# Kernel optimization log

Measured on AMD Instinct MI355X. Metric: run time of the kernel, lower is better.

Reference implementation:

```python
import jax, jax.numpy as jnp
import numpy as np

B, T, C = 4, 4096, 1024
HEAD = 128


def setup_inputs() -> dict:
    key = jax.random.key(0)
    k0, k1, k2, k3 = jax.random.split(key, 4)
    x = jax.random.normal(k0, (B, T, C), dtype=jnp.float32)
    # bias-free linear weights, stored as (in, out) so y = x @ W
    Wk = jax.random.normal(k1, (C, HEAD), dtype=jnp.float32) * (C ** -0.5)
    Wq = jax.random.normal(k2, (C, HEAD), dtype=jnp.float32) * (C ** -0.5)
    Wv = jax.random.normal(k3, (C, HEAD), dtype=jnp.float32) * (C ** -0.5)
    return {"x": x, "Wk": Wk, "Wq": Wq, "Wv": Wv}


def reference(x, Wk, Wq, Wv):
    Bx, Tx, Cx = x.shape
    k = x @ Wk            # [B,T,H]
    q = x @ Wq            # [B,T,H]
    v = x @ Wv            # [B,T,H]
    # NOTE: original code scales by C**-0.5 where C = n_embd (input dim), not head_size
    scale = Cx ** -0.5
    wei = jnp.einsum("bqh,bkh->bqk", q, k) * scale        # [B,T,T]
    causal = jnp.arange(Tx)[:, None] >= jnp.arange(Tx)[None, :]
    wei = jnp.where(causal, wei, -jnp.inf)
    wei = jax.nn.softmax(wei, axis=-1)
    # dropout rate is 0.0 in the source -> identity
    return jnp.einsum("bqk,bkh->bqh", wei, v)             # [B,T,H]
```

## Files before the change

kernel.cpp:

```cpp
#include <hip/hip_runtime.h>


typedef __bf16 bf16;
typedef bf16 bf16x8 __attribute__((ext_vector_type(8)));
typedef bf16 bf16x4 __attribute__((ext_vector_type(4)));
typedef float f32x4 __attribute__((ext_vector_type(4)));

#define L2E 1.4426950408889634f
#define TSEQ 4096
#define CDIM 1024
#define HDIM 128
#define MROWS 16384

#define GLDS(g, l)                                              \
  __builtin_amdgcn_global_load_lds(                             \
      (__attribute__((address_space(1))) void*)(g),             \
      (__attribute__((address_space(3))) void*)(l), 16, 0, 0)

static __device__ inline unsigned pkbf(float a, float b) {
  union { bf16 h; unsigned short u; } ua, ub;
  ua.h = (bf16)a; ub.h = (bf16)b;
  return ((unsigned)ub.u << 16) | (unsigned)ua.u;
}

__global__ __launch_bounds__(256) void wt_prep(const float* __restrict__ Wq,
                                               const float* __restrict__ Wk,
                                               const float* __restrict__ Wv,
                                               bf16* __restrict__ WT) {
  const int mode = blockIdx.y;
  const float* W = (mode == 0) ? Wq : (mode == 1) ? Wk : Wv;
  const int idx = blockIdx.x * 256 + threadIdx.x;
  const int n = idx >> 10;
  const int k = idx & 1023;
  WT[(size_t)mode * 131072 + idx] = (bf16)W[(size_t)k * HDIM + n];
}

__global__ __launch_bounds__(256) void qkv_gemm(const float* __restrict__ x,
                                                const bf16* __restrict__ WT,
                                                bf16* __restrict__ qb,
                                                bf16* __restrict__ kb,
                                                bf16* __restrict__ vT) {
  __shared__ __attribute__((aligned(16))) bf16 a_tile[128 * 32];
  __shared__ __attribute__((aligned(16))) bf16 b_tile[128 * 32];
  const int tid = threadIdx.x;
  const int wid = tid >> 6;
  const int lane = tid & 63;
  const int lr = lane & 15;
  const int lg = lane >> 4;
  const int wr = wid >> 1;
  const int wc = wid & 1;
  const int mode = blockIdx.y;
  const int m0 = blockIdx.x * 128;
  const bf16* wt = WT + (size_t)mode * 131072;

  int rowA[2], col8[2];
#pragma unroll
  for (int g = 0; g < 2; ++g) {
    const int idx8 = g * 256 + tid;
    rowA[g] = idx8 >> 2;
    col8[g] = (idx8 & 3) * 8;
  }

  f32x4 acc[4][4] = {};

  float4 fA[2][2];
  bf16x8 fB[2];
#pragma unroll
  for (int g = 0; g < 2; ++g) {
    const float* src = x + (size_t)(m0 + rowA[g]) * CDIM + col8[g];
    fA[g][0] = *(const float4*)src;
    fA[g][1] = *(const float4*)(src + 4);
    fB[g] = *(const bf16x8*)(wt + (size_t)rowA[g] * CDIM + col8[g]);
  }

#pragma unroll 1
  for (int kt = 0; kt < 32; ++kt) {
    __syncthreads();
#pragma unroll
    for (int g = 0; g < 2; ++g) {
      bf16x8 av;
      av[0] = (bf16)fA[g][0].x; av[1] = (bf16)fA[g][0].y;
      av[2] = (bf16)fA[g][0].z; av[3] = (bf16)fA[g][0].w;
      av[4] = (bf16)fA[g][1].x; av[5] = (bf16)fA[g][1].y;
      av[6] = (bf16)fA[g][1].z; av[7] = (bf16)fA[g][1].w;
      *(bf16x8*)&a_tile[rowA[g] * 32 + col8[g]] = av;
      *(bf16x8*)&b_tile[rowA[g] * 32 + col8[g]] = fB[g];
    }
    __syncthreads();
    if (kt + 1 < 32) {
#pragma unroll
      for (int g = 0; g < 2; ++g) {
        const float* src = x + (size_t)(m0 + rowA[g]) * CDIM + (kt + 1) * 32 + col8[g];
        fA[g][0] = *(const float4*)src;
        fA[g][1] = *(const float4*)(src + 4);
        fB[g] = *(const bf16x8*)(wt + (size_t)rowA[g] * CDIM + (kt + 1) * 32 + col8[g]);
      }
    }
    bf16x8 af[4], bfr[4];
#pragma unroll
    for (int r = 0; r < 4; ++r)
      af[r] = *(const bf16x8*)&a_tile[(wr * 64 + r * 16 + lr) * 32 + lg * 8];
#pragma unroll
    for (int c = 0; c < 4; ++c)
      bfr[c] = *(const bf16x8*)&b_tile[(wc * 64 + c * 16 + lr) * 32 + lg * 8];
#pragma unroll
    for (int r = 0; r < 4; ++r)
#pragma unroll
      for (int c = 0; c < 4; ++c)
        acc[r][c] = __builtin_amdgcn_mfma_f32_16x16x32_bf16(af[r], bfr[c], acc[r][c], 0, 0, 0);
  }

  if (mode < 2) {
    bf16* dst = (mode == 0) ? qb : kb;
    const float sc = (mode == 0) ? 0.03125f : 1.0f;
#pragma unroll
    for (int r = 0; r < 4; ++r)
#pragma unroll
      for (int c = 0; c < 4; ++c)
#pragma unroll
        for (int j = 0; j < 4; ++j) {
          const int row = m0 + wr * 64 + r * 16 + lg * 4 + j;
          const int col = wc * 64 + c * 16 + lr;
          dst[(size_t)row * HDIM + col] = (bf16)(acc[r][c][j] * sc);
        }
  } else {
#pragma unroll
    for (int r = 0; r < 4; ++r)
#pragma unroll
      for (int c = 0; c < 4; ++c) {
        const int row0 = m0 + wr * 64 + r * 16 + lg * 4;
        const int col = wc * 64 + c * 16 + lr;
        bf16x4 pv;
        pv[0] = (bf16)acc[r][c][0]; pv[1] = (bf16)acc[r][c][1];
        pv[2] = (bf16)acc[r][c][2]; pv[3] = (bf16)acc[r][c][3];
        *(bf16x4*)(vT + (size_t)(row0 >> 6) * 8192 + col * 64 + (row0 & 63)) = pv;
      }
  }
}

__global__ __launch_bounds__(512, 4) void attn_part(const bf16* __restrict__ qg,
                                                    const bf16* __restrict__ kb,
                                                    const bf16* __restrict__ vT,
                                                    bf16* __restrict__ po,
                                                    float* __restrict__ pm,
                                                    float* __restrict__ pl,
                                                    int cshift, int maxc) {
  __shared__ __attribute__((aligned(16))) char kv_lds[2][32768];
  __shared__ __attribute__((aligned(16))) bf16 p_lds[8][16][64];
  const int tid = threadIdx.x;
  const int wid = tid >> 6;
  const int lane = tid & 63;
  const int lr = lane & 15;
  const int lg = lane >> 4;

  int bx = blockIdx.x, c = blockIdx.y, b = blockIdx.z;
  if (maxc == 8) {
    const int p = blockIdx.x + 32 * (blockIdx.y + 8 * blockIdx.z);
    const int xcd = p & 7;
    const int s = p >> 3;
    const int combo = s >> 5;
    bx = s & 31;
    b = combo;
    c = (combo < 2) ? xcd : 7 - xcd;
  }

  const int qbase = bx * 128;
  const int kv0 = c << cshift;
  if (kv0 >= qbase + 128) return;
  const int kvend = min(kv0 + (1 << cshift), qbase + 128);
  const int nt = (kvend - kv0) >> 6;
  const int qr0 = qbase + wid * 16;
  const int grp = bx * 8 + wid;
  const size_t qrow = (size_t)b * TSEQ + qr0;

  const int wbase = wid * 2048;
  int ksrc[2], vsrc[2];
#pragma unroll
  for (int i = 0; i < 2; ++i) {
    const int o = wbase + i * 1024 + lane * 16;
    const int rk = o >> 8;
    ksrc[i] = rk * 256 + ((o & 255) ^ ((rk & 7) << 4));
    const int rv = o >> 7;
    vsrc[i] = rv * 128 + ((o & 127) ^ ((rv & 7) << 4));
  }
  const char* kgb = (const char*)kb + (size_t)b * TSEQ * 256;
  const char* vgb = (const char*)vT + (size_t)b * TSEQ * 256;

  const int msk = (lr & 7) << 4;
  const int m30 = (lr & 3) << 4;
  const int m6 = (lr & 4) << 4;
  const int lgx = (lg * 16) ^ m30;
  const int kreadA = lr * 256 + lgx + m6;
  const int kreadB = lr * 256 + lgx + (64 ^ m6);
  const int vreadA = 16384 + lr * 128 + lgx + m6;
  const int vreadB = 16384 + lr * 128 + lgx + (64 ^ m6);

  bf16x8 qf[4];
#pragma unroll
  for (int d = 0; d < 4; ++d)
    qf[d] = *(const bf16x8*)(qg + (qrow + lr) * HDIM + d * 32 + lg * 8);

  f32x4 o_[8] = {};
  float m_ = -1e30f, l_ = 0.0f;

  {
    const char* ks = kgb + (size_t)kv0 * 256;
    const char* vs = vgb + (size_t)kv0 * 256;
#pragma unroll
    for (int i = 0; i < 2; ++i) {
      GLDS(ks + ksrc[i], &kv_lds[0][wbase + i * 1024]);
      GLDS(vs + vsrc[i], &kv_lds[0][16384 + wbase + i * 1024]);
    }
  }
  __syncthreads();

  int cur = 0;
  for (int t = 0; t < nt; ++t) {
    const int kvt = kv0 + (t << 6);
    if (t + 1 < nt) {
      const char* ks = kgb + (size_t)(kvt + 64) * 256;
      const char* vs = vgb + (size_t)(kvt + 64) * 256;
#pragma unroll
      for (int i = 0; i < 2; ++i) {
        GLDS(ks + ksrc[i], &kv_lds[cur ^ 1][wbase + i * 1024]);
        GLDS(vs + vsrc[i], &kv_lds[cur ^ 1][16384 + wbase + i * 1024]);
      }
    }
    if (kvt < qr0 + 16) {
      const char* kbuf = kv_lds[cur];
      f32x4 s[4] = {};
      __builtin_amdgcn_s_setprio(1);
#pragma unroll
      for (int nf = 0; nf < 4; ++nf) {
        const char* kb0 = kbuf + nf * 4096;
        bf16x8 kf;
        kf = *(const bf16x8*)(kb0 + kreadA);
        s[nf] = __builtin_amdgcn_mfma_f32_16x16x32_bf16(kf, qf[0], s[nf], 0, 0, 0);
        kf = *(const bf16x8*)(kb0 + kreadB);
        s[nf] = __builtin_amdgcn_mfma_f32_16x16x32_bf16(kf, qf[1], s[nf], 0, 0, 0);
        kf = *(const bf16x8*)(kb0 + kreadA + 128);
        s[nf] = __builtin_amdgcn_mfma_f32_16x16x32_bf16(kf, qf[2], s[nf], 0, 0, 0);
        kf = *(const bf16x8*)(kb0 + kreadB + 128);
        s[nf] = __builtin_amdgcn_mfma_f32_16x16x32_bf16(kf, qf[3], s[nf], 0, 0, 0);
      }
      __builtin_amdgcn_s_setprio(0);
      if (kvt + 63 >= qr0) {
        const int q = qr0 + lr;
#pragma unroll
        for (int nf = 0; nf < 4; ++nf)
#pragma unroll
          for (int j = 0; j < 4; ++j)
            if (kvt + nf * 16 + lg * 4 + j > q) s[nf][j] = -1e30f;
      }
      float rloc = fmaxf(fmaxf(s[0][0], s[0][1]), fmaxf(s[0][2], s[0][3]));
#pragma unroll
      for (int nf = 1; nf < 4; ++nf)
        rloc = fmaxf(rloc, fmaxf(fmaxf(s[nf][0], s[nf][1]), fmaxf(s[nf][2], s[nf][3])));
      if (!__all(rloc <= m_ + 8.0f)) {
        float rmax = fmaxf(rloc, __shfl_xor(rloc, 16));
        rmax = fmaxf(rmax, __shfl_xor(rmax, 32));
        const float mn = fmaxf(m_, rmax);
        const float al = exp2f((m_ - mn) * L2E);
        m_ = mn;
        l_ *= al;
#pragma unroll
        for (int o = 0; o < 8; ++o)
#pragma unroll
          for (int j = 0; j < 4; ++j) o_[o][j] *= al;
      }
      float rsum = 0.0f;
#pragma unroll
      for (int nf = 0; nf < 4; ++nf)
#pragma unroll
        for (int j = 0; j < 4; ++j) {
          s[nf][j] = exp2f((s[nf][j] - m_) * L2E);
          rsum += s[nf][j];
        }
      l_ += rsum;
      {
        char* pw = (char*)p_lds + wid * 2048 + lr * 128;
#pragma unroll
        for (int nf = 0; nf < 4; ++nf) {
          uint2 w2;
          w2.x = pkbf(s[nf][0], s[nf][1]); w2.y = pkbf(s[nf][2], s[nf][3]);
          *(uint2*)(pw + (((nf * 32) + lg * 8) ^ msk)) = w2;
        }
      }
      asm volatile("s_waitcnt lgkmcnt(0)" ::: "memory");
      __builtin_amdgcn_sched_barrier(0);
      const char* pr = (const char*)p_lds + wid * 2048 + lr * 128;
      bf16x8 pf0 = *(const bf16x8*)(pr + lgx + m6);
      bf16x8 pf1 = *(const bf16x8*)(pr + lgx + (64 ^ m6));
      __builtin_amdgcn_s_setprio(1);
#pragma unroll
      for (int o = 0; o < 8; ++o) {
        bf16x8 vf;
        vf = *(const bf16x8*)(kbuf + vreadA + o * 2048);
        o_[o] = __builtin_amdgcn_mfma_f32_16x16x32_bf16(vf, pf0, o_[o], 0, 0, 0);
        vf = *(const bf16x8*)(kbuf + vreadB + o * 2048);
        o_[o] = __builtin_amdgcn_mfma_f32_16x16x32_bf16(vf, pf1, o_[o], 0, 0, 0);
      }
      __builtin_amdgcn_s_setprio(0);
    }
    __syncthreads();
    cur ^= 1;
  }

  l_ += __shfl_xor(l_, 16);
  l_ += __shfl_xor(l_, 32);

  const size_t slot = (size_t)(b * 256 + grp) * maxc + c;
  bf16* pob = po + slot * (16 * HDIM);
#pragma unroll
  for (int o = 0; o < 8; ++o) {
    bf16x4 pv;
    pv[0] = (bf16)o_[o][0]; pv[1] = (bf16)o_[o][1];
    pv[2] = (bf16)o_[o][2]; pv[3] = (bf16)o_[o][3];
    *(bf16x4*)(pob + lr * HDIM + o * 16 + lg * 4) = pv;
  }
  if (lg == 0) {
    pm[slot * 16 + lr] = m_;
    pl[slot * 16 + lr] = l_;
  }
}

__global__ __launch_bounds__(256) void attn_merge(const bf16* __restrict__ po,
                                                  const float* __restrict__ pm,
                                                  const float* __restrict__ pl,
                                                  float* __restrict__ out,
                                                  int cshift, int maxc) {
  const int bg = blockIdx.x;
  const int g = bg & 255;
  const int nch = ((g << 4) >> cshift) + 1;
  const int row = threadIdx.x >> 4;
  const int d8 = (threadIdx.x & 15) * 8;
  const size_t slot0 = (size_t)bg * maxc;

  float M = -1e30f;
  for (int c = 0; c < nch; ++c) M = fmaxf(M, pm[(slot0 + c) * 16 + row]);
  float L = 0.0f;
  float acc[8] = {};
  for (int c = 0; c < nch; ++c) {
    const float w = exp2f((pm[(slot0 + c) * 16 + row] - M) * L2E);
    L += w * pl[(slot0 + c) * 16 + row];
    const bf16x8 v = *(const bf16x8*)(po + (slot0 + c) * (16 * HDIM) + row * HDIM + d8);
#pragma unroll
    for (int i = 0; i < 8; ++i) acc[i] += w * (float)v[i];
  }
  const float inv = 1.0f / L;
  f32x4 r0, r1;
#pragma unroll
  for (int i = 0; i < 4; ++i) { r0[i] = acc[i] * inv; r1[i] = acc[i + 4] * inv; }
  float* dst = out + (size_t)bg * (16 * HDIM) + row * HDIM + d8;
  *(f32x4*)dst = r0;
  *(f32x4*)(dst + 4) = r1;
}

extern "C" void kernel_launch(void* const* d_in, const int* in_sizes, int n_in,
                              void* d_out, int out_size, void* d_ws, size_t ws_size,
                              hipStream_t stream) {
  const float* x  = (const float*)d_in[0];
  const float* Wk = (const float*)d_in[1];
  const float* Wq = (const float*)d_in[2];
  const float* Wv = (const float*)d_in[3];
  float* out = (float*)d_out;

  char* ws = (char*)d_ws;
  bf16* qb = (bf16*)(ws);
  bf16* kb = (bf16*)(ws + 4194304);
  bf16* vT = (bf16*)(ws + 8388608);
  bf16* WT = (bf16*)(ws + 12582912);
  const size_t pbase = 13369344;

  int cshift, maxc;
  if (ws_size >= pbase + 8ull * 1024 * 4224) { cshift = 9;  maxc = 8; }
  else if (ws_size >= pbase + 4ull * 1024 * 4224) { cshift = 10; maxc = 4; }
  else { cshift = 12; maxc = 1; }
  bf16* po = (bf16*)(ws + pbase);
  float* pm = (float*)(ws + pbase + (size_t)maxc * 1024 * 16 * 128 * 2);
  float* pl = pm + (size_t)maxc * 1024 * 16;

  wt_prep<<<dim3(512, 3), 256, 0, stream>>>(Wq, Wk, Wv, WT);
  qkv_gemm<<<dim3(128, 3), 256, 0, stream>>>(x, WT, qb, kb, vT);
  attn_part<<<dim3(32, maxc, 4), 512, 0, stream>>>(qb, kb, vT, po, pm, pl, cshift, maxc);
  attn_merge<<<1024, 256, 0, stream>>>(po, pm, pl, out, cshift, maxc);
}
```

Baseline: 90.21 us.

## Fuse Q/K/V projections into one GEMM reading x once per tile

After: 96.61 us. 1.07x slower.

```diff
diff --git a/kernel.cpp b/kernel.cpp
--- a/kernel.cpp
+++ b/kernel.cpp
@@ -35,106 +35,88 @@
   WT[(size_t)mode * 131072 + idx] = (bf16)W[(size_t)k * HDIM + n];
 }
 
-__global__ __launch_bounds__(256) void qkv_gemm(const float* __restrict__ x,
-                                                const bf16* __restrict__ WT,
-                                                bf16* __restrict__ qb,
-                                                bf16* __restrict__ kb,
-                                                bf16* __restrict__ vT) {
-  __shared__ __attribute__((aligned(16))) bf16 a_tile[128 * 32];
-  __shared__ __attribute__((aligned(16))) bf16 b_tile[128 * 32];
+__global__ __launch_bounds__(512, 2) void qkv_fused(const float* __restrict__ x,
+                                                    const bf16* __restrict__ WT,
+                                                    bf16* __restrict__ qb,
+                                                    bf16* __restrict__ kb,
+                                                    bf16* __restrict__ vT) {
+  __shared__ __attribute__((aligned(16))) bf16 a_tile[64 * 32];
+  __shared__ __attribute__((aligned(16))) bf16 b_tile[384 * 32];
   const int tid = threadIdx.x;
   const int wid = tid >> 6;
   const int lane = tid & 63;
   const int lr = lane & 15;
   const int lg = lane >> 4;
-  const int wr = wid >> 1;
-  const int wc = wid & 1;
-  const int mode = blockIdx.y;
-  const int m0 = blockIdx.x * 128;
-  const bf16* wt = WT + (size_t)mode * 131072;
-
-  int rowA[2], col8[2];
-#pragma unroll
-  for (int g = 0; g < 2; ++g) {
-    const int idx8 = g * 256 + tid;
-    rowA[g] = idx8 >> 2;
-    col8[g] = (idx8 & 3) * 8;
-  }
-
-  f32x4 acc[4][4] = {};
-
-  float4 fA[2][2];
-  bf16x8 fB[2];
-#pragma unroll
-  for (int g = 0; g < 2; ++g) {
-    const float* src = x + (size_t)(m0 + rowA[g]) * CDIM + col8[g];
-    fA[g][0] = *(const float4*)src;
-    fA[g][1] = *(const float4*)(src + 4);
-    fB[g] = *(const bf16x8*)(wt + (size_t)rowA[g] * CDIM + col8[g]);
+  const int wr = wid >> 2;
+  const int wcg = wid & 3;
+  const int m0 = blockIdx.x * 64;
+
+  const int ra = tid >> 3;
+  const int ca = (tid & 7) * 4;
+  const int rb = tid >> 2;
+  const int cb = (tid & 3) * 8;
+
+  f32x4 acc[2][6] = {};
+  float4 a0;
+  bf16x8 fB[3];
+  {
+    a0 = *(const float4*)(x + (size_t)(m0 + ra) * CDIM + ca);
+#pragma unroll
+    for (int i = 0; i < 3; ++i)
+      fB[i] = *(const bf16x8*)(WT + (size_t)i * 131072 + rb * 1024 + cb);
   }
 
 #pragma unroll 1
   for (int kt = 0; kt < 32; ++kt) {
     __syncthreads();
-#pragma unroll
-    for (int g = 0; g < 2; ++g) {
-      bf16x8 av;
-      av[0] = (bf16)fA[g][0].x; av[1] = (bf16)fA[g][0].y;
-      av[2] = (bf16)fA[g][0].z; av[3] = (bf16)fA[g][0].w;
-      av[4] = (bf16)fA[g][1].x; av[5] = (bf16)fA[g][1].y;
-      av[6] = (bf16)fA[g][1].z; av[7] = (bf16)fA[g][1].w;
-      *(bf16x8*)&a_tile[rowA[g] * 32 + col8[g]] = av;
-      *(bf16x8*)&b_tile[rowA[g] * 32 + col8[g]] = fB[g];
+    {
+      bf16x4 av;
+      av[0] = (bf16)a0.x; av[1] = (bf16)a0.y; av[2] = (bf16)a0.z; av[3] = (bf16)a0.w;
+      *(bf16x4*)&a_tile[ra * 32 + ca] = av;
+#pragma unroll
+      for (int i = 0; i < 3; ++i)
+        *(bf16x8*)&b_tile[(i * 128 + rb) * 32 + cb] = fB[i];
     }
     __syncthreads();
     if (kt + 1 < 32) {
-#pragma unroll
-      for (int g = 0; g < 2; ++g) {
-        const float* src = x + (size_t)(m0 + rowA[g]) * CDIM + (kt + 1) * 32 + col8[g];
-        fA[g][0] = *(const float4*)src;
-        fA[g][1] = *(const float4*)(src + 4);
-        fB[g] = *(const bf16x8*)(wt + (size_t)rowA[g] * CDIM + (kt + 1) * 32 + col8[g]);
-      }
-    }
-    bf16x8 af[4], bfr[4];
-#pragma unroll
-    for (int r = 0; r < 4; ++r)
-      af[r] = *(const bf16x8*)&a_tile[(wr * 64 + r * 16 + lr) * 32 + lg * 8];
-#pragma unroll
-    for (int c = 0; c < 4; ++c)
-      bfr[c] = *(const bf16x8*)&b_tile[(wc * 64 + c * 16 + lr) * 32 + lg * 8];
-#pragma unroll
-    for (int r = 0; r < 4; ++r)
-#pragma unroll
-      for (int c = 0; c < 4; ++c)
-        acc[r][c] = __builtin_amdgcn_mfma_f32_16x16x32_bf16(af[r], bfr[c], acc[r][c], 0, 0, 0);
-  }
-
-  if (mode < 2) {
-    bf16* dst = (mode == 0) ? qb : kb;
-    const float sc = (mode == 0) ? 0.03125f : 1.0f;
-#pragma unroll
-    for (int r = 0; r < 4; ++r)
-#pragma unroll
-      for (int c = 0; c < 4; ++c)
-#pragma unroll
-        for (int j = 0; j < 4; ++j) {
-          const int row = m0 + wr * 64 + r * 16 + lg * 4 + j;
-          const int col = wc * 64 + c * 16 + lr;
-          dst[(size_t)row * HDIM + col] = (bf16)(acc[r][c][j] * sc);
-        }
-  } else {
-#pragma unroll
-    for (int r = 0; r < 4; ++r)
-#pragma unroll
-      for (int c = 0; c < 4; ++c) {
-        const int row0 = m0 + wr * 64 + r * 16 + lg * 4;
-        const int col = wc * 64 + c * 16 + lr;
+      a0 = *(const float4*)(x + (size_t)(m0 + ra) * CDIM + (kt + 1) * 32 + ca);
+#pragma unroll
+      for (int i = 0; i < 3; ++i)
+        fB[i] = *(const bf16x8*)(WT + (size_t)i * 131072 + rb * 1024 + (kt + 1) * 32 + cb);
+    }
+    bf16x8 af[2];
+#pragma unroll
+    for (int r = 0; r < 2; ++r)
+      af[r] = *(const bf16x8*)&a_tile[(wr * 32 + r * 16 + lr) * 32 + lg * 8];
+#pragma unroll
+    for (int n = 0; n < 6; ++n) {
+      bf16x8 bfr = *(const bf16x8*)&b_tile[(wcg * 96 + n * 16 + lr) * 32 + lg * 8];
+      acc[0][n] = __builtin_amdgcn_mfma_f32_16x16x32_bf16(af[0], bfr, acc[0][n], 0, 0, 0);
+      acc[1][n] = __builtin_amdgcn_mfma_f32_16x16x32_bf16(af[1], bfr, acc[1][n], 0, 0, 0);
+    }
+  }
+
+#pragma unroll
+  for (int r = 0; r < 2; ++r) {
+    const int row0 = m0 + wr * 32 + r * 16 + lg * 4;
+#pragma unroll
+    for (int n = 0; n < 6; ++n) {
+      const int cg = wcg * 96 + n * 16;
+      const int mode = cg >> 7;
+      const int col = (cg & 127) + lr;
+      if (mode < 2) {
+        bf16* dst = (mode == 0) ? qb : kb;
+        const float sc = (mode == 0) ? 0.03125f : 1.0f;
+#pragma unroll
+        for (int j = 0; j < 4; ++j)
+          dst[(size_t)(row0 + j) * HDIM + col] = (bf16)(acc[r][n][j] * sc);
+      } else {
         bf16x4 pv;
-        pv[0] = (bf16)acc[r][c][0]; pv[1] = (bf16)acc[r][c][1];
-        pv[2] = (bf16)acc[r][c][2]; pv[3] = (bf16)acc[r][c][3];
+        pv[0] = (bf16)acc[r][n][0]; pv[1] = (bf16)acc[r][n][1];
+        pv[2] = (bf16)acc[r][n][2]; pv[3] = (bf16)acc[r][n][3];
         *(bf16x4*)(vT + (size_t)(row0 >> 6) * 8192 + col * 64 + (row0 & 63)) = pv;
       }
+    }
   }
 }
 
@@ -381,7 +363,7 @@
   float* pl = pm + (size_t)maxc * 1024 * 16;
 
   wt_prep<<<dim3(512, 3), 256, 0, stream>>>(Wq, Wk, Wv, WT);
-  qkv_gemm<<<dim3(128, 3), 256, 0, stream>>>(x, WT, qb, kb, vT);
+  qkv_fused<<<256, 512, 0, stream>>>(x, WT, qb, kb, vT);
   attn_part<<<dim3(32, maxc, 4), 512, 0, stream>>>(qb, kb, vT, po, pm, pl, cshift, maxc);
   attn_merge<<<1024, 256, 0, stream>>>(po, pm, pl, out, cshift, maxc);
 }
```
